# Performance work log

Measured on AMD Instinct MI355X. Metric: run time of the kernel, lower is better.

The kernel has to match this reference:

```python
import jax, jax.numpy as jnp
import numpy as np

FACTOR = 5

def setup_inputs() -> dict:
    key = jax.random.key(0)
    k1, k2, k3 = jax.random.split(key, 3)
    B, L, H, D = 4, 2048, 8, 64
    logL = int(np.ceil(np.log(L)))          # 8
    U_part = min(2 * FACTOR * logL, L)      # 80 sampled keys per query
    queries = jax.random.normal(k1, (B, L, H, D), dtype=jnp.float32)
    keys = jax.random.normal(k2, (B, L, H, D), dtype=jnp.float32)
    index_sample = jax.random.randint(k3, (L, U_part), 0, L)
    return {"queries": queries, "keys": keys, "index_sample": index_sample}

def reference(queries, keys, index_sample):
    B, L, H, D = queries.shape
    q = jnp.transpose(queries, (0, 2, 1, 3))   # [B,H,L,D]
    k = jnp.transpose(keys, (0, 2, 1, 3))      # [B,H,L,D]
    logL = int(np.ceil(np.log(L)))
    u = min(FACTOR * logL, L)                  # n_top queries

    # sample keys per query position: [B,H,L,S,D]
    K_sample = k[:, :, index_sample, :]
    # Q_i . K_sample_ij : [B,H,L,S]
    QK_sample = jnp.einsum('bhld,bhlsd->bhls', q, K_sample)
    # sparsity measure M = max - mean (mean over full L as in source)
    M = QK_sample.max(axis=-1) - QK_sample.sum(axis=-1) / L   # [B,H,L]
    _, M_top = jax.lax.top_k(M, u)                            # [B,H,u]

    # gather selected queries and compute full scores against all keys
    Q_reduce = jnp.take_along_axis(q, M_top[..., None], axis=2)  # [B,H,u,D]
    scale = 1.0 / jnp.sqrt(jnp.float32(D))
    scores = jnp.einsum('bhud,bhld->bhul', Q_reduce, k) * scale  # [B,H,u,L]
    attn = jax.nn.softmax(scores, axis=-1)

    # scatter softmaxed rows into full [B,H,L,L] attention matrix (rest zeros)
    out = jnp.zeros((B, H, L, L), dtype=attn.dtype)
    b_idx = jnp.arange(B)[:, None, None]
    h_idx = jnp.arange(H)[None, :, None]
    out = out.at[b_idx, h_idx, M_top, :].set(attn)
    return out
```

## Files before the change

### kernel.cpp

```cpp
#include <hip/hip_runtime.h>
#include <math.h>

#define NB 4
#define NL 2048
#define NH 8
#define ND 64
#define NUPART 80
#define NUTOP 40
#define ZROWS_K1 320
#define NZB_PER_BH 432
#define NATTN (NB * NH * NUTOP)

typedef float vfloat4 __attribute__((ext_vector_type(4)));

__global__ __launch_bounds__(256) void k_compute_M_zero(
    const float* __restrict__ q, const float* __restrict__ k,
    const int* __restrict__ idx, float* __restrict__ M,
    float* __restrict__ out)
{
    const int t = threadIdx.x;

    {
        const int bhz = blockIdx.x >> 9;
        const int j   = blockIdx.x & 511;
        vfloat4* o = (vfloat4*)out + (size_t)bhz * (NL * NL / 4) + j * 320 + t;
        const vfloat4 z = (vfloat4)(0.0f);
        o[0] = z;
        if (t < 64) o[256] = z;
    }

    const int w    = blockIdx.x * 4 + (t >> 6);
    const int lane = t & 63;
    const int l    = w & (NL - 1);
    const int bh   = w >> 11;
    const int h    = bh & (NH - 1);
    const int b    = bh >> 3;
    const int sl   = lane >> 2;
    const int dg   = lane & 3;
    const int d0   = dg * 16;

    const float4* qv = (const float4*)(q + (((size_t)(b * NL + l) * NH + h) * ND + d0));
    const float4 q0 = qv[0], q1 = qv[1], q2 = qv[2], q3 = qv[3];

    float mx = -INFINITY, sm = 0.0f;
#pragma unroll
    for (int r = 0; r < 5; ++r) {
        const int s  = r * 16 + sl;
        const int ki = idx[l * NUPART + s];
        const float4* kv = (const float4*)(k + (((size_t)(b * NL + ki) * NH + h) * ND + d0));
        const float4 k0 = kv[0], k1 = kv[1], k2 = kv[2], k3 = kv[3];
        float p = q0.x * k0.x + q0.y * k0.y + q0.z * k0.z + q0.w * k0.w
                + q1.x * k1.x + q1.y * k1.y + q1.z * k1.z + q1.w * k1.w
                + q2.x * k2.x + q2.y * k2.y + q2.z * k2.z + q2.w * k2.w
                + q3.x * k3.x + q3.y * k3.y + q3.z * k3.z + q3.w * k3.w;
        p += __shfl_xor(p, 1);
        p += __shfl_xor(p, 2);
        mx = fmaxf(mx, p);
        sm += p;
    }
#pragma unroll
    for (int m = 4; m < 64; m <<= 1) {
        mx = fmaxf(mx, __shfl_xor(mx, m));
        sm += __shfl_xor(sm, m);
    }
    if (lane == 0) M[w] = mx - sm * (1.0f / (float)NL);
}

__global__ __launch_bounds__(256) void k_topk(
    const float* __restrict__ M, int* __restrict__ rowmap,
    int* __restrict__ Mtop)
{
    __shared__ float sM[NL];
    __shared__ float rv[4];
    __shared__ int   ri[4];
    const int bh = blockIdx.x;
    const int t  = threadIdx.x;

    for (int j = t; j < NL; j += 256) {
        sM[j] = M[bh * NL + j];
        rowmap[bh * NL + j] = 0;
    }
    __syncthreads();

    for (int it = 0; it < NUTOP; ++it) {
        float v = -INFINITY;
        int   i = NL;
        for (int j = t; j < NL; j += 256) {
            const float m = sM[j];
            if (m > v || (m == v && j < i)) { v = m; i = j; }
        }
#pragma unroll
        for (int off = 1; off < 64; off <<= 1) {
            const float ov = __shfl_xor(v, off);
            const int   oi = __shfl_xor(i, off);
            if (ov > v || (ov == v && oi < i)) { v = ov; i = oi; }
        }
        const int wid = t >> 6;
        if ((t & 63) == 0) { rv[wid] = v; ri[wid] = i; }
        __syncthreads();
        if (t == 0) {
            for (int w2 = 1; w2 < 4; ++w2) {
                if (rv[w2] > v || (rv[w2] == v && ri[w2] < i)) { v = rv[w2]; i = ri[w2]; }
            }
            Mtop[bh * NUTOP + it] = i;
            rowmap[bh * NL + i] = 1;
            sM[i] = -INFINITY;
        }
        __syncthreads();
    }
}

__global__ __launch_bounds__(256) void k_attn_zero(
    const float* __restrict__ q, const float* __restrict__ k,
    const int* __restrict__ rowmap, const int* __restrict__ Mtop,
    float* __restrict__ out)
{
    const int t = threadIdx.x;

    if (blockIdx.x >= NATTN) {
        const int zb = blockIdx.x - NATTN;
        const int bh = zb / NZB_PER_BH;
        const int ri = zb - bh * NZB_PER_BH;
        const int r0 = ZROWS_K1 + ri * 4;
        const vfloat4 z = (vfloat4)(0.0f);
#pragma unroll
        for (int rr = 0; rr < 4; ++rr) {
            const int r = r0 + rr;
            if (rowmap[bh * NL + r]) continue;
            vfloat4* o = (vfloat4*)out + ((size_t)bh * NL + r) * (NL / 4) + t;
            o[0]   = z;
            o[256] = z;
        }
        return;
    }

    const int bh  = blockIdx.x / NUTOP;
    const int ui  = blockIdx.x % NUTOP;
    const int b   = bh >> 3;
    const int h   = bh & 7;
    const int row = Mtop[bh * NUTOP + ui];

    __shared__ float redm[4];
    __shared__ float reds[4];
    const int lane = t & 63;
    const int wid  = t >> 6;

    const float4* qv = (const float4*)(q + (((size_t)(b * NL + row)) * NH + h) * ND);
    float4 qr[16];
#pragma unroll
    for (int i = 0; i < 16; ++i) qr[i] = qv[i];

    float sc[8];
    float mx = -INFINITY;
#pragma unroll
    for (int j = 0; j < 8; ++j) {
        const int l = t + 256 * j;
        const float4* kv = (const float4*)(k + (((size_t)(b * NL + l)) * NH + h) * ND);
        float s = 0.0f;
#pragma unroll
        for (int i = 0; i < 16; ++i) {
            const float4 kk = kv[i];
            s += qr[i].x * kk.x + qr[i].y * kk.y + qr[i].z * kk.z + qr[i].w * kk.w;
        }
        sc[j] = s * 0.125f;
        mx = fmaxf(mx, sc[j]);
    }

#pragma unroll
    for (int off = 1; off < 64; off <<= 1) mx = fmaxf(mx, __shfl_xor(mx, off));
    if (lane == 0) redm[wid] = mx;
    __syncthreads();
    mx = fmaxf(fmaxf(redm[0], redm[1]), fmaxf(redm[2], redm[3]));

    float lsum = 0.0f;
#pragma unroll
    for (int j = 0; j < 8; ++j) {
        sc[j] = __expf(sc[j] - mx);
        lsum += sc[j];
    }
#pragma unroll
    for (int off = 1; off < 64; off <<= 1) lsum += __shfl_xor(lsum, off);
    if (lane == 0) reds[wid] = lsum;
    __syncthreads();
    const float inv = 1.0f / (reds[0] + reds[1] + reds[2] + reds[3]);

    float* orow = out + ((size_t)bh * NL + row) * NL;
#pragma unroll
    for (int j = 0; j < 8; ++j) {
        orow[t + 256 * j] = sc[j] * inv;
    }
}

extern "C" void kernel_launch(void* const* d_in, const int* in_sizes, int n_in,
                              void* d_out, int out_size, void* d_ws, size_t ws_size,
                              hipStream_t stream) {
    const float* q   = (const float*)d_in[0];
    const float* k   = (const float*)d_in[1];
    const int*   idx = (const int*)d_in[2];
    float* out = (float*)d_out;

    float* Mws    = (float*)d_ws;
    int*   rowmap = (int*)((char*)d_ws + (size_t)NB * NH * NL * 4);
    int*   Mtop   = (int*)((char*)d_ws + (size_t)NB * NH * NL * 8);

    k_compute_M_zero<<<NB * NH * NL / 4, 256, 0, stream>>>(q, k, idx, Mws, out);
    k_topk<<<NB * NH, 256, 0, stream>>>(Mws, rowmap, Mtop);
    k_attn_zero<<<NATTN + NB * NH * NZB_PER_BH, 256, 0, stream>>>(q, k, rowmap, Mtop, out);
}
```

Baseline: 403.4 us.

## Split score GEMM into column-tiled kernel with K reuse, fuse softmax into zero pass

Moves the QK^T scores for the selected rows into a separate kernel where each thread holds one key column in registers and loops over all 40 cached queries from shared memory. This replaces 40 blocks per head that each re-read all of K. The zero-fill split is also reworked: the first kernel zeroes a contiguous 12288-row prefix (384 float4 per block), and the last kernel zeroes the remaining rows and runs the softmax on the precomputed scores. This adds one kernel launch and a workspace round trip for the scores.

```diff
diff --git a/kernel.cpp b/kernel.cpp
--- a/kernel.cpp
+++ b/kernel.cpp
@@ -7,11 +7,20 @@
 #define ND 64
 #define NUPART 80
 #define NUTOP 40
-#define ZROWS_K1 320
-#define NZB_PER_BH 432
+#define NROWS (NB * NH * NL)
 #define NATTN (NB * NH * NUTOP)
+#define Z1ROWS 12288
+#define NZ3 (NROWS - Z1ROWS)
+#define K3BLK (NZ3 / 4)
 
 typedef float vfloat4 __attribute__((ext_vector_type(4)));
+
+__device__ __forceinline__ void zero_row(float* __restrict__ out, int r, int t) {
+    vfloat4* o = (vfloat4*)out + (size_t)r * (NL / 4) + t;
+    const vfloat4 z = (vfloat4)(0.0f);
+    o[0]   = z;
+    o[256] = z;
+}
 
 __global__ __launch_bounds__(256) void k_compute_M_zero(
     const float* __restrict__ q, const float* __restrict__ k,
@@ -21,12 +30,10 @@
     const int t = threadIdx.x;
 
     {
-        const int bhz = blockIdx.x >> 9;
-        const int j   = blockIdx.x & 511;
-        vfloat4* o = (vfloat4*)out + (size_t)bhz * (NL * NL / 4) + j * 320 + t;
+        vfloat4* o = (vfloat4*)out + (size_t)blockIdx.x * 384 + t;
         const vfloat4 z = (vfloat4)(0.0f);
         o[0] = z;
-        if (t < 64) o[256] = z;
+        if (t < 128) o[256] = z;
     }
 
     const int w    = blockIdx.x * 4 + (t >> 6);
@@ -110,84 +117,99 @@
     }
 }
 
-__global__ __launch_bounds__(256) void k_attn_zero(
+__global__ __launch_bounds__(256) void k_scores(
     const float* __restrict__ q, const float* __restrict__ k,
+    const int* __restrict__ Mtop, float* __restrict__ scores)
+{
+    __shared__ float4 qs[NUTOP][16];
+    __shared__ int    rows[NUTOP];
+
+    const int bh = blockIdx.x >> 3;
+    const int ct = blockIdx.x & 7;
+    const int b  = bh >> 3;
+    const int h  = bh & 7;
+    const int t  = threadIdx.x;
+
+    if (t < NUTOP) rows[t] = Mtop[bh * NUTOP + t];
+    __syncthreads();
+    for (int i = t; i < NUTOP * 16; i += 256) {
+        const int r = i >> 4, d = i & 15;
+        qs[r][d] = ((const float4*)q)[((size_t)(b * NL + rows[r]) * NH + h) * 16 + d];
+    }
+    __syncthreads();
+
+    const int c = ct * 256 + t;
+    const float4* kv = (const float4*)k + ((size_t)(b * NL + c) * NH + h) * 16;
+    float4 kc[16];
+#pragma unroll
+    for (int i = 0; i < 16; ++i) kc[i] = kv[i];
+
+    float* srow = scores + (size_t)bh * NUTOP * NL + c;
+    for (int r = 0; r < NUTOP; ++r) {
+        float s = 0.0f;
+#pragma unroll
+        for (int i = 0; i < 16; ++i) {
+            const float4 qq = qs[r][i];
+            s += qq.x * kc[i].x + qq.y * kc[i].y + qq.z * kc[i].z + qq.w * kc[i].w;
+        }
+        srow[(size_t)r * NL] = s * 0.125f;
+    }
+}
+
+__global__ __launch_bounds__(256) void k_zero_attn(
     const int* __restrict__ rowmap, const int* __restrict__ Mtop,
-    float* __restrict__ out)
+    const float* __restrict__ scores, float* __restrict__ out)
 {
     const int t = threadIdx.x;
 
-    if (blockIdx.x >= NATTN) {
-        const int zb = blockIdx.x - NATTN;
-        const int bh = zb / NZB_PER_BH;
-        const int ri = zb - bh * NZB_PER_BH;
-        const int r0 = ZROWS_K1 + ri * 4;
-        const vfloat4 z = (vfloat4)(0.0f);
+    {
+        const int r0 = Z1ROWS + blockIdx.x * 4;
 #pragma unroll
         for (int rr = 0; rr < 4; ++rr) {
             const int r = r0 + rr;
-            if (rowmap[bh * NL + r]) continue;
-            vfloat4* o = (vfloat4*)out + ((size_t)bh * NL + r) * (NL / 4) + t;
-            o[0]   = z;
-            o[256] = z;
-        }
-        return;
-    }
-
-    const int bh  = blockIdx.x / NUTOP;
-    const int ui  = blockIdx.x % NUTOP;
-    const int b   = bh >> 3;
-    const int h   = bh & 7;
-    const int row = Mtop[bh * NUTOP + ui];
-
-    __shared__ float redm[4];
-    __shared__ float reds[4];
-    const int lane = t & 63;
-    const int wid  = t >> 6;
-
-    const float4* qv = (const float4*)(q + (((size_t)(b * NL + row)) * NH + h) * ND);
-    float4 qr[16];
-#pragma unroll
-    for (int i = 0; i < 16; ++i) qr[i] = qv[i];
-
-    float sc[8];
-    float mx = -INFINITY;
-#pragma unroll
-    for (int j = 0; j < 8; ++j) {
-        const int l = t + 256 * j;
-        const float4* kv = (const float4*)(k + (((size_t)(b * NL + l)) * NH + h) * ND);
-        float s = 0.0f;
-#pragma unroll
-        for (int i = 0; i < 16; ++i) {
-            const float4 kk = kv[i];
-            s += qr[i].x * kk.x + qr[i].y * kk.y + qr[i].z * kk.z + qr[i].w * kk.w;
-        }
-        sc[j] = s * 0.125f;
-        mx = fmaxf(mx, sc[j]);
-    }
-
-#pragma unroll
-    for (int off = 1; off < 64; off <<= 1) mx = fmaxf(mx, __shfl_xor(mx, off));
-    if (lane == 0) redm[wid] = mx;
-    __syncthreads();
-    mx = fmaxf(fmaxf(redm[0], redm[1]), fmaxf(redm[2], redm[3]));
-
-    float lsum = 0.0f;
-#pragma unroll
-    for (int j = 0; j < 8; ++j) {
-        sc[j] = __expf(sc[j] - mx);
-        lsum += sc[j];
-    }
-#pragma unroll
-    for (int off = 1; off < 64; off <<= 1) lsum += __shfl_xor(lsum, off);
-    if (lane == 0) reds[wid] = lsum;
-    __syncthreads();
-    const float inv = 1.0f / (reds[0] + reds[1] + reds[2] + reds[3]);
-
-    float* orow = out + ((size_t)bh * NL + row) * NL;
-#pragma unroll
-    for (int j = 0; j < 8; ++j) {
-        orow[t + 256 * j] = sc[j] * inv;
+            if (!rowmap[r]) zero_row(out, r, t);
+        }
+    }
+
+    if (blockIdx.x < NATTN) {
+        __shared__ float redm[4];
+        __shared__ float reds[4];
+        const int a    = blockIdx.x;
+        const int bh   = a / NUTOP;
+        const int ui   = a % NUTOP;
+        const int row  = Mtop[bh * NUTOP + ui];
+        const int lane = t & 63;
+        const int wid  = t >> 6;
+
+        const float* srow = scores + ((size_t)bh * NUTOP + ui) * NL;
+        float sc[8];
+        float mx = -INFINITY;
+#pragma unroll
+        for (int j = 0; j < 8; ++j) {
+            sc[j] = srow[t + 256 * j];
+            mx = fmaxf(mx, sc[j]);
+        }
+#pragma unroll
+        for (int off = 1; off < 64; off <<= 1) mx = fmaxf(mx, __shfl_xor(mx, off));
+        if (lane == 0) redm[wid] = mx;
+        __syncthreads();
+        mx = fmaxf(fmaxf(redm[0], redm[1]), fmaxf(redm[2], redm[3]));
+
+        float lsum = 0.0f;
+#pragma unroll
+        for (int j = 0; j < 8; ++j) {
+            sc[j] = __expf(sc[j] - mx);
+            lsum += sc[j];
+        }
+#pragma unroll
+        for (int off = 1; off < 64; off <<= 1) lsum += __shfl_xor(lsum, off);
+        if (lane == 0) reds[wid] = lsum;
+        __syncthreads();
+        const float inv = 1.0f / (reds[0] + reds[1] + reds[2] + reds[3]);
+
+        float* orow = out + ((size_t)bh * NL + row) * NL;
+#pragma unroll
+        for (int j = 0; j < 8; ++j) orow[t + 256 * j] = sc[j] * inv;
     }
 }
 
@@ -200,10 +222,12 @@
     float* out = (float*)d_out;
 
     float* Mws    = (float*)d_ws;
-    int*   rowmap = (int*)((char*)d_ws + (size_t)NB * NH * NL * 4);
-    int*   Mtop   = (int*)((char*)d_ws + (size_t)NB * NH * NL * 8);
-
-    k_compute_M_zero<<<NB * NH * NL / 4, 256, 0, stream>>>(q, k, idx, Mws, out);
+    int*   rowmap = (int*)((char*)d_ws + (256 << 10));
+    int*   Mtop   = (int*)((char*)d_ws + (512 << 10));
+    float* scores = (float*)((char*)d_ws + (1 << 20));
+
+    k_compute_M_zero<<<NROWS / 4, 256, 0, stream>>>(q, k, idx, Mws, out);
     k_topk<<<NB * NH, 256, 0, stream>>>(Mws, rowmap, Mtop);
-    k_attn_zero<<<NATTN + NB * NH * NZB_PER_BH, 256, 0, stream>>>(q, k, rowmap, Mtop, out);
-}
+    k_scores<<<NB * NH * 8, 256, 0, stream>>>(q, k, Mtop, scores);
+    k_zero_attn<<<K3BLK, 256, 0, stream>>>(rowmap, Mtop, scores, out);
+}
```

New measurement: 345.1 us. -14.5%, faster.
